# Optimization experiments

Hardware: AMD Instinct MI355X
Metric: run time of the kernel (lower is better)

Reference implementation:

```python
import jax, jax.numpy as jnp
import numpy as np

N_USERS = 50000
N_ITEMS = 100000
N = N_USERS + N_ITEMS
D = 64
N_LAYERS = 3
N_INTENTS = 128
T_SIZE = 32
TEMP = 0.2
KL_REG = 0.01
EMB_REG = 1e-5
INT_REG = 1e-5
SSL_REG = 0.1
B = 4096
E_RAND = 3_000_000


def setup_inputs() -> dict:
    key = jax.random.key(0)
    ks = jax.random.split(key, 12)
    # edge list: random edges + self loops so every node has degree >= 1
    h_rand = jax.random.randint(ks[0], (E_RAND,), 0, N, dtype=jnp.int32)
    t_rand = jax.random.randint(ks[1], (E_RAND,), 0, N, dtype=jnp.int32)
    loops = jnp.arange(N, dtype=jnp.int32)
    h_list = jnp.concatenate([loops, h_rand])
    t_list = jnp.concatenate([loops, t_rand])
    return {
        "user_emb": jax.random.normal(ks[2], (N_USERS, D), jnp.float32) * 0.1,
        "item_emb": jax.random.normal(ks[3], (N_ITEMS, D), jnp.float32) * 0.1,
        "user_intent": jax.random.normal(ks[4], (D, N_INTENTS), jnp.float32) * 0.1,
        "item_intent": jax.random.normal(ks[5], (D, N_INTENTS), jnp.float32) * 0.1,
        "lin_w": jax.random.normal(ks[6], (D, T_SIZE), jnp.float32) * 0.1,
        "lin_b": jnp.zeros((D,), jnp.float32),
        "eps": jax.random.uniform(ks[7], (N, D), jnp.float32),
        "h_list": h_list,
        "t_list": t_list,
        "users": jax.random.randint(ks[8], (B,), 0, N_USERS, dtype=jnp.int32),
        "pos_items": jax.random.randint(ks[9], (B,), 0, N_ITEMS, dtype=jnp.int32),
        "neg_items": jax.random.randint(ks[10], (B,), 0, N_ITEMS, dtype=jnp.int32),
    }


def _normalize(x):
    return x / jnp.linalg.norm(x, axis=1, keepdims=True)


def _infonce(e1, e2):
    pos = jnp.exp(jnp.sum(e1 * e2, axis=1) / TEMP)                 # [B]
    neg = jnp.sum(jnp.exp(e1 @ e2.T / TEMP), axis=1)               # [B]
    return jnp.mean(-jnp.log(pos / (neg + 1e-8) + 1e-8))


def reference(user_emb, item_emb, user_intent, item_intent, lin_w, lin_b,
              eps, h_list, t_list, users, pos_items, neg_items):
    # ---- symmetric normalization D^-1/2 A D^-1/2 (A values = 1) ----
    deg = jax.ops.segment_sum(jnp.ones_like(h_list, dtype=jnp.float32), h_list,
                              num_segments=N)
    d_inv = deg ** -0.5
    g_vals = d_inv[h_list] * d_inv[t_list]                          # [E]

    # ---- multi-layer SpMM propagation, layer-sum aggregation ----
    ego = jnp.concatenate([user_emb, item_emb], axis=0)             # [N, D]
    acc = ego
    cur = ego
    for _ in range(N_LAYERS):
        cur = jax.ops.segment_sum(g_vals[:, None] * cur[t_list], h_list,
                                  num_segments=N)                   # spmm
        acc = acc + cur
    all_emb = acc                                                   # [N, D]
    ua, ia = all_emb[:N_USERS], all_emb[N_USERS:]

    # ---- generative learning ----
    mean = all_emb
    std = jax.nn.softplus(all_emb[:, :T_SIZE])
    std = std @ lin_w.T + lin_b + 1e-8                              # [N, D]
    gen_emb = mean + eps * std

    # ---- intent model ----
    u_int = jax.nn.softmax(ua @ user_intent, axis=1) @ user_intent.T
    i_int = jax.nn.softmax(ia @ item_intent, axis=1) @ item_intent.T

    # ---- BPR loss ----
    u_e = ua[users]
    pos_scores = jnp.sum(u_e * ia[pos_items], axis=1)
    neg_scores = jnp.sum(u_e * ia[neg_items], axis=1)
    bpr_loss = jnp.mean(jax.nn.softplus(neg_scores - pos_scores))

    # ---- KL loss ----
    kl = -0.5 * (1.0 + 2.0 * std - jnp.square(mean) - jnp.exp(2.0 * std))
    kl = jnp.where(jnp.isfinite(kl), kl, 0.0)
    kl_loss = KL_REG * jnp.mean(jnp.sum(kl, axis=1))
    gen_loss = bpr_loss + kl_loss

    # ---- embedding / intent regularizers ----
    emb_loss = EMB_REG * (jnp.sum(jnp.square(user_emb[users]))
                          + jnp.sum(jnp.square(item_emb[pos_items]))
                          + jnp.sum(jnp.square(item_emb[neg_items])))
    int_loss = INT_REG * (jnp.sum(jnp.square(user_intent))
                          + jnp.sum(jnp.square(item_intent)))

    # ---- SSL (InfoNCE) loss ----
    u_gen = _normalize(gen_emb[:N_USERS][users])
    i_gen = _normalize(gen_emb[N_USERS:][pos_items])
    u_i = _normalize(u_int[users])
    i_i = _normalize(i_int[pos_items])
    cl_loss = SSL_REG * (_infonce(u_gen, u_i) + _infonce(i_gen, i_i))

    return (gen_loss, cl_loss, emb_loss, int_loss)
```

## Files before the change

### kernel.cpp

```cpp
#include <hip/hip_runtime.h>

#define NU 50000
#define NI 100000
#define NT 150000
#define BB 4096
#define NBUCK 147
#define BCAP 24576
#define NCH 8
#define KLB 1920

typedef __attribute__((ext_vector_type(8))) short bf16x8;
typedef __attribute__((ext_vector_type(4))) float f32x4;
typedef __attribute__((ext_vector_type(2))) float f32x2;
typedef unsigned long long u64;

__device__ __forceinline__ float softplusf(float x) {
  return fmaxf(x, 0.f) + __logf(1.f + __expf(-fabsf(x)));
}
__device__ __forceinline__ float wsum(float v) {
#pragma unroll
  for (int o = 32; o > 0; o >>= 1) v += __shfl_xor(v, o, 64);
  return v;
}
__device__ __forceinline__ unsigned short f2b(float x) {
  unsigned u = __float_as_uint(x);
  return (unsigned short)((u + 0x7FFFu + ((u >> 16) & 1u)) >> 16);
}
__device__ __forceinline__ float b2f(unsigned us) {
  return __uint_as_float(us << 16);
}
__device__ __forceinline__ float bfe(bf16x8 v, int j) {
  return __uint_as_float(((unsigned)(unsigned short)v[j]) << 16);
}
__device__ __forceinline__ void unp4(u64 v, float* o) {
  unsigned lo = (unsigned)v, hi = (unsigned)(v >> 32);
  o[0] = __uint_as_float(lo << 16);
  o[1] = __uint_as_float(lo & 0xffff0000u);
  o[2] = __uint_as_float(hi << 16);
  o[3] = __uint_as_float(hi & 0xffff0000u);
}
__device__ __forceinline__ u64 pk4(float x0, float x1, float x2, float x3) {
  return (u64)((unsigned)f2b(x0) | ((unsigned)f2b(x1) << 16)) |
         ((u64)((unsigned)f2b(x2) | ((unsigned)f2b(x3) << 16)) << 32);
}
__device__ __forceinline__ f32x2 pkfma(f32x2 a, f32x2 b, f32x2 c) {
  f32x2 d;
  asm("v_pk_fma_f32 %0, %1, %2, %3" : "=v"(d) : "v"(a), "v"(b), "v"(c));
  return d;
}

__global__ void k_zero(int* __restrict__ gcur, float* __restrict__ negu,
                       float* __restrict__ negi) {
  int t = threadIdx.x;
  for (int i = t; i < NBUCK; i += 256) gcur[i] = 0;
  for (int i = t; i < BB; i += 256) { negu[i] = 0.f; negi[i] = 0.f; }
}

__global__ __launch_bounds__(256) void k_part(const int* __restrict__ h,
                                              const int* __restrict__ t,
                                              int* __restrict__ gcur,
                                              uint2* __restrict__ part, int E) {
  __shared__ int cnt[NBUCK];
  __shared__ int base[NBUCK];
  for (int b = threadIdx.x; b < NBUCK; b += 256) cnt[b] = 0;
  __syncthreads();
  int e0 = blockIdx.x * 4096 + threadIdx.x * 16;
  int nval = E - e0;
  nval = nval < 0 ? 0 : (nval > 16 ? 16 : nval);
  int hh[16], tt[16];
  if (nval == 16) {
    const int4* hp = (const int4*)(h + e0);
    const int4* tp = (const int4*)(t + e0);
#pragma unroll
    for (int j = 0; j < 4; j++) {
      int4 v = hp[j];
      hh[j * 4] = v.x; hh[j * 4 + 1] = v.y; hh[j * 4 + 2] = v.z; hh[j * 4 + 3] = v.w;
      int4 w = tp[j];
      tt[j * 4] = w.x; tt[j * 4 + 1] = w.y; tt[j * 4 + 2] = w.z; tt[j * 4 + 3] = w.w;
    }
  } else {
    for (int j = 0; j < nval; j++) { hh[j] = h[e0 + j]; tt[j] = t[e0 + j]; }
  }
  for (int j = 0; j < nval; j++) atomicAdd(&cnt[hh[j] >> 10], 1);
  __syncthreads();
  for (int b = threadIdx.x; b < NBUCK; b += 256) {
    int c = cnt[b];
    base[b] = c ? atomicAdd(&gcur[b], c) : 0;
    cnt[b] = 0;
  }
  __syncthreads();
  for (int j = 0; j < nval; j++) {
    int b = hh[j] >> 10;
    int r = atomicAdd(&cnt[b], 1);
    uint2 v; v.x = (unsigned)hh[j]; v.y = (unsigned)tt[j];
    part[(size_t)b * BCAP + base[b] + r] = v;
  }
}

__global__ __launch_bounds__(256) void k_count2(const uint2* __restrict__ part,
                                                const int* __restrict__ gcur,
                                                int* __restrict__ cnt_chunk) {
  __shared__ int hist[1024];
  int b = blockIdx.x, c = blockIdx.y, tid = threadIdx.x;
  for (int i = tid; i < 1024; i += 256) hist[i] = 0;
  __syncthreads();
  int m = gcur[b];
  int lo = (int)(((long long)m * c) >> 3);
  int hi = (int)(((long long)m * (c + 1)) >> 3);
  const uint2* pp = part + (size_t)b * BCAP;
  for (int i = lo + tid; i < hi; i += 256) atomicAdd(&hist[pp[i].x & 1023], 1);
  __syncthreads();
  for (int i = tid; i < 1024; i += 256)
    cnt_chunk[((((size_t)b << 10) + i) << 3) + c] = hist[i];
}

__global__ __launch_bounds__(256) void k_node(int* __restrict__ cnt_chunk,
                                              int* __restrict__ rloc_g,
                                              float* __restrict__ d_inv,
                                              int* __restrict__ btot) {
  __shared__ int sd[256];
  int b = blockIdx.x, tid = threadIdx.x;
  int n0 = b << 10;
  int pd[4];
  int s = 0;
#pragma unroll
  for (int j = 0; j < 4; j++) {
    int idx = tid * 4 + j;
    size_t base = ((size_t)(n0 + idx)) << 3;
    int run = 0;
#pragma unroll
    for (int c = 0; c < NCH; c++) {
      int v = cnt_chunk[base + c];
      cnt_chunk[base + c] = run;
      run += v;
    }
    int n = n0 + idx;
    if (n < NT) {
      d_inv[n] = 1.0f / sqrtf((float)run);
      pd[j] = run;
    } else pd[j] = 0;
    s += pd[j];
  }
  sd[tid] = s;
  __syncthreads();
  for (int o = 1; o < 256; o <<= 1) {
    int x = (tid >= o) ? sd[tid - o] : 0;
    __syncthreads();
    sd[tid] += x;
    __syncthreads();
  }
  int run2 = sd[tid] - s;
#pragma unroll
  for (int j = 0; j < 4; j++) {
    int idx = tid * 4 + j, n = n0 + idx;
    if (n < NT) rloc_g[n] = run2;
    run2 += pd[j];
  }
  if (tid == 255) btot[b] = sd[255];
}

__global__ __launch_bounds__(256) void k_fill2(const uint2* __restrict__ part,
                                               const int* __restrict__ gcur,
                                               const int* __restrict__ chunkpre,
                                               const int* __restrict__ rloc_g,
                                               const int* __restrict__ btot,
                                               const float* __restrict__ d_inv,
                                               uint2* __restrict__ edges,
                                               int* __restrict__ row_ptr) {
  __shared__ int curs[1024];
  __shared__ float dl[1024];
  __shared__ int sd[256];
  __shared__ int exs[256];
  int b = blockIdx.x, c = blockIdx.y, tid = threadIdx.x;
  int v = (tid < NBUCK) ? btot[tid] : 0;
  sd[tid] = v;
  __syncthreads();
  for (int o = 1; o < 256; o <<= 1) {
    int x = (tid >= o) ? sd[tid - o] : 0;
    __syncthreads();
    sd[tid] += x;
    __syncthreads();
  }
  exs[tid] = sd[tid] - v;
  __syncthreads();
  int exB = exs[b];
  int n0 = b << 10;
  for (int i = tid; i < 1024; i += 256) {
    int n = n0 + i;
    if (n < NT) {
      int rp = exB + rloc_g[n];
      curs[i] = rp + chunkpre[((((size_t)b << 10) + i) << 3) + c];
      dl[i] = d_inv[n];
      if (c == 0) row_ptr[n] = rp;
    }
  }
  if (c == 0 && b == 0 && tid == 0) row_ptr[NT] = exs[255];
  __syncthreads();
  int m = gcur[b];
  int lo = (int)(((long long)m * c) >> 3);
  int hi = (int)(((long long)m * (c + 1)) >> 3);
  const uint2* pp = part + (size_t)b * BCAP;
  for (int i = lo + tid; i < hi; i += 256) {
    uint2 pe = pp[i];
    int slot = atomicAdd(&curs[pe.x & 1023], 1);
    float g = dl[pe.x & 1023] * d_inv[pe.y];
    uint2 w; w.x = pe.y; w.y = __float_as_uint(g);
    edges[slot] = w;
  }
}

__global__ void k_init(const float4* __restrict__ ue, const float4* __restrict__ ie,
                       unsigned* __restrict__ cur, u64* __restrict__ acc64,
                       int nU4, int nTot4) {
  int i = blockIdx.x * 256 + threadIdx.x;
  if (i >= nTot4) return;
  float4 v = (i < nU4) ? ue[i] : ie[i - nU4];
  int p = __builtin_amdgcn_cvt_pk_fp8_f32(v.x, v.y, 0, false);
  p = __builtin_amdgcn_cvt_pk_fp8_f32(v.z, v.w, p, true);
  cur[i] = (unsigned)p;
  acc64[i] = pk4(v.x, v.y, v.z, v.w);
}

__device__ __forceinline__ void agg32(const u64* __restrict__ ep,
                                      const unsigned* __restrict__ cur,
                                      int i, int e, int d, int b4,
                                      f32x2& a01, f32x2& a23) {
  int ia = i + d;
  int ib = ia + 16;
  u64 ra = ep[ia < e ? ia : e - 1];
  u64 rb = ep[ib < e ? ib : e - 1];
  unsigned rax = (unsigned)ra;
  unsigned ray = (ia < e) ? (unsigned)(ra >> 32) : 0u;
  unsigned rbx = (unsigned)rb;
  unsigned rby = (ib < e) ? (unsigned)(rb >> 32) : 0u;
  unsigned iA0 = __shfl(rax, b4 + 0, 64); float gA0 = __uint_as_float(__shfl(ray, b4 + 0, 64));
  unsigned iA1 = __shfl(rax, b4 + 1, 64); float gA1 = __uint_as_float(__shfl(ray, b4 + 1, 64));
  unsigned iA2 = __shfl(rax, b4 + 2, 64); float gA2 = __uint_as_float(__shfl(ray, b4 + 2, 64));
  unsigned iA3 = __shfl(rax, b4 + 3, 64); float gA3 = __uint_as_float(__shfl(ray, b4 + 3, 64));
  unsigned vA0 = cur[(iA0 << 4) + (unsigned)d];
  unsigned vA1 = cur[(iA1 << 4) + (unsigned)d];
  unsigned vA2 = cur[(iA2 << 4) + (unsigned)d];
  unsigned vA3 = cur[(iA3 << 4) + (unsigned)d];
  unsigned iB0 = __shfl(rbx, b4 + 0, 64); float gB0 = __uint_as_float(__shfl(rby, b4 + 0, 64));
  unsigned iB1 = __shfl(rbx, b4 + 1, 64); float gB1 = __uint_as_float(__shfl(rby, b4 + 1, 64));
  unsigned iB2 = __shfl(rbx, b4 + 2, 64); float gB2 = __uint_as_float(__shfl(rby, b4 + 2, 64));
  unsigned iB3 = __shfl(rbx, b4 + 3, 64); float gB3 = __uint_as_float(__shfl(rby, b4 + 3, 64));
  unsigned vB0 = cur[(iB0 << 4) + (unsigned)d];
  unsigned vB1 = cur[(iB1 << 4) + (unsigned)d];
  unsigned vB2 = cur[(iB2 << 4) + (unsigned)d];
  unsigned vB3 = cur[(iB3 << 4) + (unsigned)d];
  f32x2 g2;
  g2.x = gA0; g2.y = gA0;
  a01 = pkfma(__builtin_amdgcn_cvt_pk_f32_fp8(vA0, false), g2, a01);
  a23 = pkfma(__builtin_amdgcn_cvt_pk_f32_fp8(vA0, true), g2, a23);
  g2.x = gA1; g2.y = gA1;
  a01 = pkfma(__builtin_amdgcn_cvt_pk_f32_fp8(vA1, false), g2, a01);
  a23 = pkfma(__builtin_amdgcn_cvt_pk_f32_fp8(vA1, true), g2, a23);
  g2.x = gA2; g2.y = gA2;
  a01 = pkfma(__builtin_amdgcn_cvt_pk_f32_fp8(vA2, false), g2, a01);
  a23 = pkfma(__builtin_amdgcn_cvt_pk_f32_fp8(vA2, true), g2, a23);
  g2.x = gA3; g2.y = gA3;
  a01 = pkfma(__builtin_amdgcn_cvt_pk_f32_fp8(vA3, false), g2, a01);
  a23 = pkfma(__builtin_amdgcn_cvt_pk_f32_fp8(vA3, true), g2, a23);
  g2.x = gB0; g2.y = gB0;
  a01 = pkfma(__builtin_amdgcn_cvt_pk_f32_fp8(vB0, false), g2, a01);
  a23 = pkfma(__builtin_amdgcn_cvt_pk_f32_fp8(vB0, true), g2, a23);
  g2.x = gB1; g2.y = gB1;
  a01 = pkfma(__builtin_amdgcn_cvt_pk_f32_fp8(vB1, false), g2, a01);
  a23 = pkfma(__builtin_amdgcn_cvt_pk_f32_fp8(vB1, true), g2, a23);
  g2.x = gB2; g2.y = gB2;
  a01 = pkfma(__builtin_amdgcn_cvt_pk_f32_fp8(vB2, false), g2, a01);
  a23 = pkfma(__builtin_amdgcn_cvt_pk_f32_fp8(vB2, true), g2, a23);
  g2.x = gB3; g2.y = gB3;
  a01 = pkfma(__builtin_amdgcn_cvt_pk_f32_fp8(vB3, false), g2, a01);
  a23 = pkfma(__builtin_amdgcn_cvt_pk_f32_fp8(vB3, true), g2, a23);
}

__global__ __launch_bounds__(256) void k_agg(const int* __restrict__ row_ptr,
                                             const uint2* __restrict__ edges,
                                             const unsigned* __restrict__ cur,
                                             unsigned* __restrict__ nxt,
                                             u64* __restrict__ acc64,
                                             int last) {
  int node0 = (((blockIdx.x << 2) + (threadIdx.x >> 6)) << 1);
  int node1 = node0 + 1;
  unsigned lane = threadIdx.x & 63;
  int d = (int)(lane & 15);
  int g = (int)(lane >> 4);
  int b4 = g << 2;
  int s0 = row_ptr[node0];
  int e0 = row_ptr[node1];
  int e1 = row_ptr[node1 + 1];
  int s1 = e0;
  f32x2 x01 = {0.f, 0.f}, x23 = {0.f, 0.f};
  f32x2 y01 = {0.f, 0.f}, y23 = {0.f, 0.f};
  const u64* ep = (const u64*)edges;
  int l0 = e0 - s0, l1 = e1 - s1;
  int len = l0 > l1 ? l0 : l1;
  for (int k = 0; k < len; k += 32) {
    agg32(ep, cur, s0 + k, e0, d, b4, x01, x23);
    agg32(ep, cur, s1 + k, e1, d, b4, y01, y23);
  }
  float x0 = x01.x, x1 = x01.y, x2 = x23.x, x3 = x23.y;
  float y0 = y01.x, y1 = y01.y, y2 = y23.x, y3 = y23.y;
  x0 += __shfl_xor(x0, 16, 64); x1 += __shfl_xor(x1, 16, 64);
  x2 += __shfl_xor(x2, 16, 64); x3 += __shfl_xor(x3, 16, 64);
  y0 += __shfl_xor(y0, 16, 64); y1 += __shfl_xor(y1, 16, 64);
  y2 += __shfl_xor(y2, 16, 64); y3 += __shfl_xor(y3, 16, 64);
  x0 += __shfl_xor(x0, 32, 64); x1 += __shfl_xor(x1, 32, 64);
  x2 += __shfl_xor(x2, 32, 64); x3 += __shfl_xor(x3, 32, 64);
  y0 += __shfl_xor(y0, 32, 64); y1 += __shfl_xor(y1, 32, 64);
  y2 += __shfl_xor(y2, 32, 64); y3 += __shfl_xor(y3, 32, 64);
  if (g < 2) {
    int nd = (g == 0) ? node0 : node1;
    float a0 = (g == 0) ? x0 : y0;
    float a1 = (g == 0) ? x1 : y1;
    float a2 = (g == 0) ? x2 : y2;
    float a3 = (g == 0) ? x3 : y3;
    unsigned ro = ((unsigned)nd << 4) + (unsigned)d;
    u64 pv = acc64[ro];
    unsigned lo32 = (unsigned)pv, hi32 = (unsigned)(pv >> 32);
    float z0 = __uint_as_float(lo32 << 16) + a0;
    float z1 = __uint_as_float(lo32 & 0xffff0000u) + a1;
    float z2 = __uint_as_float(hi32 << 16) + a2;
    float z3 = __uint_as_float(hi32 & 0xffff0000u) + a3;
    acc64[ro] = pk4(z0, z1, z2, z3);
  } else if (!last) {
    int nd = (g == 2) ? node0 : node1;
    float a0 = (g == 2) ? x0 : y0;
    float a1 = (g == 2) ? x1 : y1;
    float a2 = (g == 2) ? x2 : y2;
    float a3 = (g == 2) ? x3 : y3;
    unsigned ro = ((unsigned)nd << 4) + (unsigned)d;
    int p = __builtin_amdgcn_cvt_pk_fp8_f32(a0, a1, 0, false);
    p = __builtin_amdgcn_cvt_pk_fp8_f32(a2, a3, p, true);
    nxt[ro] = (unsigned)p;
  }
}

__global__ __launch_bounds__(256) void k_batch(
    const unsigned short* __restrict__ accB,
    const float* __restrict__ user_emb, const float* __restrict__ item_emb,
    const float* __restrict__ eps,
    const float* __restrict__ user_int, const float* __restrict__ item_int,
    const float* __restrict__ lin_w, const float* __restrict__ lin_b,
    const int* __restrict__ users, const int* __restrict__ pos_items,
    const int* __restrict__ neg_items,
    unsigned short* __restrict__ ugen_b, unsigned short* __restrict__ uio_b,
    unsigned short* __restrict__ igen_b, unsigned short* __restrict__ iio_b,
    float* __restrict__ posu, float* __restrict__ posi,
    double* __restrict__ bprp, double* __restrict__ esp) {
  __shared__ __align__(16) unsigned short sUIT[128 * 72];
  __shared__ __align__(16) unsigned short sUI[64 * 136];
  __shared__ __align__(16) unsigned short sP[4][16 * 136];
  __shared__ double red[8];
  int bid = blockIdx.x;
  int lane = threadIdx.x & 63;
  int wid = threadIdx.x >> 6;
  int n = lane & 15, q = lane >> 4;
  int isI = bid >> 6;
  int i0 = ((bid & 63) << 6) + wid * 16;
  const float* intent = isI ? item_int : user_int;
  for (int i = threadIdx.x; i < 8192; i += 256) {
    int dd = i >> 7, kk = i & 127;
    unsigned short v = f2b(intent[i]);
    sUIT[kk * 72 + dd] = v;
    sUI[dd * 136 + kk] = v;
  }
  __syncthreads();
  unsigned short* myP = &sP[wid][0];
  int piN = pos_items[i0 + n];
  int rw = isI ? (NU + piN) : users[i0 + n];
  const unsigned short* arp = accB + (size_t)rw * 64;
  bf16x8 a0 = *(const bf16x8*)(arp + q * 8);
  bf16x8 a1 = *(const bf16x8*)(arp + 32 + q * 8);
  f32x4 c[8];
#pragma unroll
  for (int kt = 0; kt < 8; kt++) {
    const unsigned short* bp = &sUIT[(kt * 16 + n) * 72 + q * 8];
    bf16x8 b0 = *(const bf16x8*)bp;
    bf16x8 b1 = *(const bf16x8*)(bp + 32);
    f32x4 z = {0.f, 0.f, 0.f, 0.f};
    z = __builtin_amdgcn_mfma_f32_16x16x32_bf16(a0, b0, z, 0, 0, 0);
    c[kt] = __builtin_amdgcn_mfma_f32_16x16x32_bf16(a1, b1, z, 0, 0, 0);
  }
  float mx[4], tot[4];
#pragma unroll
  for (int r = 0; r < 4; r++) {
    float m = c[0][r];
#pragma unroll
    for (int kt = 1; kt < 8; kt++) m = fmaxf(m, c[kt][r]);
#pragma unroll
    for (int o = 1; o < 16; o <<= 1) m = fmaxf(m, __shfl_xor(m, o, 64));
    mx[r] = m;
  }
#pragma unroll
  for (int kt = 0; kt < 8; kt++)
#pragma unroll
    for (int r = 0; r < 4; r++) c[kt][r] = __expf(c[kt][r] - mx[r]);
#pragma unroll
  for (int r = 0; r < 4; r++) {
    float t = 0.f;
#pragma unroll
    for (int kt = 0; kt < 8; kt++) t += c[kt][r];
#pragma unroll
    for (int o = 1; o < 16; o <<= 1) t += __shfl_xor(t, o, 64);
    tot[r] = 1.f / t;
  }
#pragma unroll
  for (int kt = 0; kt < 8; kt++)
#pragma unroll
    for (int r = 0; r < 4; r++)
      myP[(q * 4 + r) * 136 + kt * 16 + n] = f2b(c[kt][r] * tot[r]);
  f32x4 s[4];
#pragma unroll
  for (int dt = 0; dt < 4; dt++) s[dt] = (f32x4){0.f, 0.f, 0.f, 0.f};
#pragma unroll
  for (int cc = 0; cc < 4; cc++) {
    bf16x8 pa = *(const bf16x8*)&myP[n * 136 + cc * 32 + q * 8];
#pragma unroll
    for (int dt = 0; dt < 4; dt++) {
      bf16x8 bb = *(const bf16x8*)&sUI[(dt * 16 + n) * 136 + cc * 32 + q * 8];
      s[dt] = __builtin_amdgcn_mfma_f32_16x16x32_bf16(pa, bb, s[dt], 0, 0, 0);
    }
  }
  float rin[4];
#pragma unroll
  for (int r = 0; r < 4; r++) {
    float t = 0.f;
#pragma unroll
    for (int dt = 0; dt < 4; dt++) t += s[dt][r] * s[dt][r];
#pragma unroll
    for (int o = 1; o < 16; o <<= 1) t += __shfl_xor(t, o, 64);
    rin[r] = 1.f / sqrtf(t);
  }
  float iov[4][4];
  unsigned short* iob = isI ? iio_b : uio_b;
#pragma unroll
  for (int dt = 0; dt < 4; dt++)
#pragma unroll
    for (int r = 0; r < 4; r++) {
      float v = s[dt][r] * rin[r];
      iov[dt][r] = v;
      iob[(size_t)(i0 + q * 4 + r) * 64 + dt * 16 + n] = f2b(v);
    }
  bf16x8 A3;
#pragma unroll
  for (int j = 0; j < 8; j++) A3[j] = (short)f2b(softplusf(bfe(a0, j)));
  f32x4 sd4[4];
  float lbv[4];
#pragma unroll
  for (int dt = 0; dt < 4; dt++) {
    const float* wp = lin_w + (size_t)(dt * 16 + n) * 32 + q * 8;
    float4 w0 = *(const float4*)wp;
    float4 w1 = *(const float4*)(wp + 4);
    bf16x8 B3;
    B3[0] = (short)f2b(w0.x); B3[1] = (short)f2b(w0.y);
    B3[2] = (short)f2b(w0.z); B3[3] = (short)f2b(w0.w);
    B3[4] = (short)f2b(w1.x); B3[5] = (short)f2b(w1.y);
    B3[6] = (short)f2b(w1.z); B3[7] = (short)f2b(w1.w);
    f32x4 z = {0.f, 0.f, 0.f, 0.f};
    sd4[dt] = __builtin_amdgcn_mfma_f32_16x16x32_bf16(A3, B3, z, 0, 0, 0);
    lbv[dt] = lin_b[dt * 16 + n];
  }
  *(bf16x8*)&myP[n * 136 + q * 8] = a0;
  *(bf16x8*)&myP[n * 136 + 32 + q * 8] = a1;
  int rwr[4];
#pragma unroll
  for (int r = 0; r < 4; r++) rwr[r] = __shfl(rw, q * 4 + r, 64);
  float ge[4][4];
#pragma unroll
  for (int dt = 0; dt < 4; dt++)
#pragma unroll
    for (int r = 0; r < 4; r++) {
      float mcv = b2f(myP[(q * 4 + r) * 136 + dt * 16 + n]);
      float ep = eps[(size_t)rwr[r] * 64 + dt * 16 + n];
      float sdf = sd4[dt][r] + lbv[dt] + 1e-8f;
      ge[dt][r] = mcv + ep * sdf;
    }
  float gin[4];
#pragma unroll
  for (int r = 0; r < 4; r++) {
    float t = 0.f;
#pragma unroll
    for (int dt = 0; dt < 4; dt++) t += ge[dt][r] * ge[dt][r];
#pragma unroll
    for (int o = 1; o < 16; o <<= 1) t += __shfl_xor(t, o, 64);
    gin[r] = 1.f / sqrtf(t);
  }
  float pd[4] = {0.f, 0.f, 0.f, 0.f};
  unsigned short* gob = isI ? igen_b : ugen_b;
#pragma unroll
  for (int dt = 0; dt < 4; dt++)
#pragma unroll
    for (int r = 0; r < 4; r++) {
      float go = ge[dt][r] * gin[r];
      gob[(size_t)(i0 + q * 4 + r) * 64 + dt * 16 + n] = f2b(go);
      pd[r] = fmaf(go, iov[dt][r], pd[r]);
    }
  float* posX = isI ? posi : posu;
#pragma unroll
  for (int r = 0; r < 4; r++) {
    float t = pd[r];
#pragma unroll
    for (int o = 1; o < 16; o <<= 1) t += __shfl_xor(t, o, 64);
    if (n == 0) posX[i0 + q * 4 + r] = t;
  }
  if (!isI) {
    int niN = neg_items[i0 + n];
    const unsigned short* pp = accB + (size_t)(NU + piN) * 64;
    const unsigned short* np = accB + (size_t)(NU + niN) * 64;
    bf16x8 p0 = *(const bf16x8*)(pp + q * 8);
    bf16x8 p1 = *(const bf16x8*)(pp + 32 + q * 8);
    bf16x8 n0 = *(const bf16x8*)(np + q * 8);
    bf16x8 n1 = *(const bf16x8*)(np + 32 + q * 8);
    float ps = 0.f, ns = 0.f;
#pragma unroll
    for (int j = 0; j < 8; j++) {
      float m0 = bfe(a0, j), m1 = bfe(a1, j);
      ps = fmaf(m0, bfe(p0, j), ps); ps = fmaf(m1, bfe(p1, j), ps);
      ns = fmaf(m0, bfe(n0, j), ns); ns = fmaf(m1, bfe(n1, j), ns);
    }
    ps += __shfl_xor(ps, 16, 64); ps += __shfl_xor(ps, 32, 64);
    ns += __shfl_xor(ns, 16, 64); ns += __shfl_xor(ns, 32, 64);
    float bpr = softplusf(ns - ps);
    const float* uep = user_emb + (size_t)rw * 64 + q * 16;
    float es = 0.f;
#pragma unroll
    for (int j = 0; j < 4; j++) {
      float4 u4 = *(const float4*)(uep + j * 4);
      es += u4.x * u4.x + u4.y * u4.y + u4.z * u4.z + u4.w * u4.w;
    }
    es += __shfl_xor(es, 16, 64); es += __shfl_xor(es, 32, 64);
#pragma unroll
    for (int o = 1; o < 16; o <<= 1) {
      bpr += __shfl_xor(bpr, o, 64);
      es += __shfl_xor(es, o, 64);
    }
    if (lane == 0) { red[wid] = (double)bpr; red[4 + wid] = (double)es; }
    __syncthreads();
    if (threadIdx.x == 0) {
      bprp[bid] = red[0] + red[1] + red[2] + red[3];
      esp[bid] = red[4] + red[5] + red[6] + red[7];
    }
  } else {
    int niN = neg_items[i0 + n];
    const float* pe = item_emb + (size_t)piN * 64 + q * 16;
    const float* ne = item_emb + (size_t)niN * 64 + q * 16;
    float es = 0.f;
#pragma unroll
    for (int j = 0; j < 4; j++) {
      float4 u4 = *(const float4*)(pe + j * 4);
      float4 v4 = *(const float4*)(ne + j * 4);
      es += u4.x * u4.x + u4.y * u4.y + u4.z * u4.z + u4.w * u4.w;
      es += v4.x * v4.x + v4.y * v4.y + v4.z * v4.z + v4.w * v4.w;
    }
    es += __shfl_xor(es, 16, 64); es += __shfl_xor(es, 32, 64);
#pragma unroll
    for (int o = 1; o < 16; o <<= 1) es += __shfl_xor(es, o, 64);
    if (lane == 0) red[wid] = (double)es;
    __syncthreads();
    if (threadIdx.x == 0)
      esp[bid] = red[0] + red[1] + red[2] + red[3];
  }
}

__global__ __launch_bounds__(256) void k_nk(
    const unsigned short* __restrict__ e1u, const unsigned short* __restrict__ e2u,
    const unsigned short* __restrict__ e1i, const unsigned short* __restrict__ e2i,
    float* __restrict__ negu, float* __restrict__ negi,
    const unsigned short* __restrict__ accB,
    const float* __restrict__ lin_w, const float* __restrict__ lin_b,
    const float* __restrict__ user_int, const float* __restrict__ item_int,
    double* __restrict__ klp, double* __restrict__ intp) {
  __shared__ double red[4];
  __shared__ __align__(16) uint4 sE2[2048];
  int bid = blockIdx.x;
  int lane = threadIdx.x & 63;
  int wid = threadIdx.x >> 6;
  int n = lane & 15, q = lane >> 4;
  if (bid < 2048) {
    int bx = bid & 63, by = bid >> 6;
    int pr = by >> 4, jq = by & 15;
    const unsigned short* e1 = pr ? e1i : e1u;
    const unsigned short* e2 = pr ? e2i : e2u;
    float* nego = pr ? negi : negu;
    const uint4* e2v = (const uint4*)e2 + (size_t)jq * 2048;
#pragma unroll
    for (int k = 0; k < 8; k++) {
      int i = (int)threadIdx.x + k * 256;
      int row = i >> 3, cch = i & 7;
      sE2[(i & ~7) | (cch ^ (row & 7))] = e2v[i];
    }
    int i0 = bx * 64 + wid * 16;
    const bf16x8* arow = (const bf16x8*)(e1 + (size_t)(i0 + n) * 64 + q * 8);
    bf16x8 a0 = arow[0];
    bf16x8 a1 = arow[4];
    __syncthreads();
    f32x4 accv = {0.f, 0.f, 0.f, 0.f};
    int sw = n & 7;
    for (int jt = 0; jt < 16; jt += 2) {
      int r0 = jt * 16 + n;
      const uint4* base0 = &sE2[r0 * 8];
      const uint4* base1 = &sE2[(r0 + 16) * 8];
      bf16x8 b0 = *(const bf16x8*)&base0[q ^ sw];
      bf16x8 b1 = *(const bf16x8*)&base0[(q + 4) ^ sw];
      bf16x8 b2 = *(const bf16x8*)&base1[q ^ sw];
      bf16x8 b3 = *(const bf16x8*)&base1[(q + 4) ^ sw];
      f32x4 c = {0.f, 0.f, 0.f, 0.f};
      f32x4 c2 = {0.f, 0.f, 0.f, 0.f};
      c = __builtin_amdgcn_mfma_f32_16x16x32_bf16(a0, b0, c, 0, 0, 0);
      c = __builtin_amdgcn_mfma_f32_16x16x32_bf16(a1, b1, c, 0, 0, 0);
      c2 = __builtin_amdgcn_mfma_f32_16x16x32_bf16(a0, b2, c2, 0, 0, 0);
      c2 = __builtin_amdgcn_mfma_f32_16x16x32_bf16(a1, b3, c2, 0, 0, 0);
#pragma unroll
      for (int r = 0; r < 4; r++)
        accv[r] += __expf(5.0f * c[r]) + __expf(5.0f * c2[r]);
    }
#pragma unroll
    for (int o = 1; o < 16; o <<= 1) {
#pragma unroll
      for (int r = 0; r < 4; r++) accv[r] += __shfl_xor(accv[r], o, 64);
    }
    if (n == 0) {
#pragma unroll
      for (int r = 0; r < 4; r++) atomicAdd(&nego[i0 + q * 4 + r], accv[r]);
    }
  } else if (bid < 2048 + KLB) {
    bf16x8 B0, B1, B2, B3;
    float lb0, lb1, lb2, lb3;
    {
      const float* w0 = lin_w + (0 * 16 + n) * 32 + q * 8;
      const float* w1 = lin_w + (1 * 16 + n) * 32 + q * 8;
      const float* w2 = lin_w + (2 * 16 + n) * 32 + q * 8;
      const float* w3 = lin_w + (3 * 16 + n) * 32 + q * 8;
#pragma unroll
      for (int j = 0; j < 8; j++) {
        B0[j] = (short)f2b(w0[j]);
        B1[j] = (short)f2b(w1[j]);
        B2[j] = (short)f2b(w2[j]);
        B3[j] = (short)f2b(w3[j]);
      }
      lb0 = lin_b[0 * 16 + n] + 1e-8f;
      lb1 = lin_b[1 * 16 + n] + 1e-8f;
      lb2 = lin_b[2 * 16 + n] + 1e-8f;
      lb3 = lin_b[3 * 16 + n] + 1e-8f;
    }
    const int TI = NT / 16;
    int w0id = (bid - 2048) * 4 + wid;
    int nwv = KLB * 4;
    double dsum = 0.0;
    for (int tile = w0id; tile < TI; tile += nwv) {
      const uint4* rp = (const uint4*)(accB + (size_t)(tile * 16 + n) * 64 + q * 8);
      uint4 A = rp[0];
      uint4 C = rp[4];
      u64 A0 = ((u64)A.y << 32) | A.x;
      u64 A1 = ((u64)A.w << 32) | A.z;
      u64 C0 = ((u64)C.y << 32) | C.x;
      u64 C1 = ((u64)C.w << 32) | C.z;
      float av[8], bv[8];
      unp4(A0, av); unp4(A1, av + 4);
      unp4(C0, bv); unp4(C1, bv + 4);
      float msum = 0.f;
#pragma unroll
      for (int j = 0; j < 8; j++) msum += av[j] * av[j] + bv[j] * bv[j];
      bf16x8 Af;
#pragma unroll
      for (int j = 0; j < 8; j++) Af[j] = (short)f2b(softplusf(av[j]));
      f32x4 z = {0.f, 0.f, 0.f, 0.f};
      f32x4 c0 = __builtin_amdgcn_mfma_f32_16x16x32_bf16(Af, B0, z, 0, 0, 0);
      f32x4 c1 = __builtin_amdgcn_mfma_f32_16x16x32_bf16(Af, B1, z, 0, 0, 0);
      f32x4 c2 = __builtin_amdgcn_mfma_f32_16x16x32_bf16(Af, B2, z, 0, 0, 0);
      f32x4 c3 = __builtin_amdgcn_mfma_f32_16x16x32_bf16(Af, B3, z, 0, 0, 0);
      float ksum = 0.f;
#pragma unroll
      for (int r = 0; r < 4; r++) {
        float s0 = c0[r] + lb0, s1 = c1[r] + lb1, s2 = c2[r] + lb2, s3 = c3[r] + lb3;
        ksum += -0.5f * (1.f + 2.f * s0 - __expf(2.f * s0));
        ksum += -0.5f * (1.f + 2.f * s1 - __expf(2.f * s1));
        ksum += -0.5f * (1.f + 2.f * s2 - __expf(2.f * s2));
        ksum += -0.5f * (1.f + 2.f * s3 - __expf(2.f * s3));
      }
      dsum += (double)wsum(ksum + 0.5f * msum);
    }
    if (lane == 0) red[wid] = dsum;
    __syncthreads();
    if (threadIdx.x == 0)
      klp[bid - 2048] = red[0] + red[1] + red[2] + red[3];
  } else {
    float s = 0.f;
    for (int i = threadIdx.x; i < 64 * 128; i += 256) {
      float a = user_int[i], b = item_int[i];
      s = fmaf(a, a, s);
      s = fmaf(b, b, s);
    }
    s = wsum(s);
    if (lane == 0) red[wid] = (double)s;
    __syncthreads();
    if (threadIdx.x == 0)
      intp[0] = red[0] + red[1] + red[2] + red[3];
  }
}

__global__ __launch_bounds__(256) void k_out(
    const float* __restrict__ posu, const float* __restrict__ posi,
    const float* __restrict__ negu, const float* __restrict__ negi,
    const double* __restrict__ bprp, const double* __restrict__ esp,
    const double* __restrict__ klp, const double* __restrict__ intp,
    float* __restrict__ out) {
  __shared__ double redd[16];
  int tid = threadIdx.x;
  int lane = tid & 63, wid = tid >> 6;
  double cl = 0.0;
  for (int i = tid; i < 2 * BB; i += 256) {
    int pr = i >> 12, idx = i & (BB - 1);
    float ng = pr ? negi[idx] : negu[idx];
    float dt = pr ? posi[idx] : posu[idx];
    float pos = expf(5.0f * dt);
    cl += (double)(-logf(pos / (ng + 1e-8f) + 1e-8f));
  }
  double kl = 0.0;
  for (int i = tid; i < KLB; i += 256) kl += klp[i];
  double bpr = (tid < 64) ? bprp[tid] : 0.0;
  double es = (tid < 128) ? esp[tid] : 0.0;
#pragma unroll
  for (int o = 32; o > 0; o >>= 1) {
    cl += __shfl_xor(cl, o, 64);
    kl += __shfl_xor(kl, o, 64);
    bpr += __shfl_xor(bpr, o, 64);
    es += __shfl_xor(es, o, 64);
  }
  if (lane == 0) {
    redd[wid] = cl; redd[4 + wid] = kl;
    redd[8 + wid] = bpr; redd[12 + wid] = es;
  }
  __syncthreads();
  if (tid == 0) {
    double cls = redd[0] + redd[1] + redd[2] + redd[3];
    double kls = redd[4] + redd[5] + redd[6] + redd[7];
    double bprs = redd[8] + redd[9] + redd[10] + redd[11];
    double ess = redd[12] + redd[13] + redd[14] + redd[15];
    out[0] = (float)(bprs / (double)BB + 0.01 * kls / (double)NT);
    out[1] = (float)(0.1 * cls / (double)BB);
    out[2] = (float)(1e-5 * ess);
    out[3] = (float)(1e-5 * intp[0]);
  }
}

extern "C" void kernel_launch(void* const* d_in, const int* in_sizes, int n_in,
                              void* d_out, int out_size, void* d_ws, size_t ws_size,
                              hipStream_t stream) {
  const float* user_emb = (const float*)d_in[0];
  const float* item_emb = (const float*)d_in[1];
  const float* user_int = (const float*)d_in[2];
  const float* item_int = (const float*)d_in[3];
  const float* lin_w = (const float*)d_in[4];
  const float* lin_b = (const float*)d_in[5];
  const float* eps = (const float*)d_in[6];
  const int* h_list = (const int*)d_in[7];
  const int* t_list = (const int*)d_in[8];
  const int* users = (const int*)d_in[9];
  const int* pos_items = (const int*)d_in[10];
  const int* neg_items = (const int*)d_in[11];
  float* out = (float*)d_out;
  const int E = in_sizes[7];

  char* ws = (char*)d_ws;
  size_t off = 0;
  auto take = [&](size_t bytes) -> char* {
    char* p = ws + off;
    off = (off + bytes + 255) & ~(size_t)255;
    return p;
  };
  int* row_ptr = (int*)take((size_t)(NT + 1) * 4);
  float* d_inv = (float*)take((size_t)NT * 4);
  int* rloc_g = (int*)take((size_t)NT * 4);
  int* cnt_chunk = (int*)take((size_t)NBUCK * NCH * 1024 * 4);
  int* gcur = (int*)take(NBUCK * 4);
  int* btot = (int*)take(NBUCK * 4);
  uint2* edges = (uint2*)take((size_t)E * 8);
  unsigned* bufA = (unsigned*)take((size_t)NT * 16 * 4);
  unsigned* bufB = (unsigned*)take((size_t)NT * 16 * 4);
  unsigned short* accB = (unsigned short*)take((size_t)NBUCK * BCAP * 8);
  unsigned short* ugen_b = (unsigned short*)take((size_t)BB * 64 * 2);
  unsigned short* igen_b = (unsigned short*)take((size_t)BB * 64 * 2);
  unsigned short* uio_b = (unsigned short*)take((size_t)BB * 64 * 2);
  unsigned short* iio_b = (unsigned short*)take((size_t)BB * 64 * 2);
  float* posu = (float*)take((size_t)BB * 4);
  float* posi = (float*)take((size_t)BB * 4);
  float* negu = (float*)take((size_t)BB * 4);
  float* negi = (float*)take((size_t)BB * 4);
  double* klp = (double*)take((size_t)KLB * 8);
  double* bprp = (double*)take(64 * 8);
  double* esp = (double*)take(128 * 8);
  double* intp = (double*)take(8);
  if (off > ws_size) return;
  uint2* part = (uint2*)accB;
  u64* acc64 = (u64*)accB;

  k_zero<<<1, 256, 0, stream>>>(gcur, negu, negi);

  int gridP = (E + 4095) / 4096;
  k_part<<<gridP, 256, 0, stream>>>(h_list, t_list, gcur, part, E);
  k_count2<<<dim3(NBUCK, NCH), 256, 0, stream>>>(part, gcur, cnt_chunk);
  k_node<<<NBUCK, 256, 0, stream>>>(cnt_chunk, rloc_g, d_inv, btot);
  k_fill2<<<dim3(NBUCK, NCH), 256, 0, stream>>>(part, gcur, cnt_chunk, rloc_g,
                                                btot, d_inv, edges, row_ptr);

  int nU4 = NU * 16, nTot4 = NT * 16;
  k_init<<<(nTot4 + 255) / 256, 256, 0, stream>>>((const float4*)user_emb,
                                                  (const float4*)item_emb, bufA,
                                                  acc64, nU4, nTot4);
  int gridAgg = NT / 8;
  k_agg<<<gridAgg, 256, 0, stream>>>(row_ptr, edges, bufA, bufB, acc64, 0);
  k_agg<<<gridAgg, 256, 0, stream>>>(row_ptr, edges, bufB, bufA, acc64, 0);
  k_agg<<<gridAgg, 256, 0, stream>>>(row_ptr, edges, bufA, bufB, acc64, 1);

  k_batch<<<128, 256, 0, stream>>>(accB, user_emb, item_emb, eps,
                                   user_int, item_int, lin_w, lin_b,
                                   users, pos_items, neg_items,
                                   ugen_b, uio_b, igen_b, iio_b,
                                   posu, posi, bprp, esp);
  k_nk<<<2048 + KLB + 1, 256, 0, stream>>>(ugen_b, uio_b, igen_b, iio_b,
                                           negu, negi, accB, lin_w, lin_b,
                                           user_int, item_int, klp, intp);
  k_out<<<1, 256, 0, stream>>>(posu, posi, negu, negi, bprp, esp, klp, intp,
                               out);
}
```

Before: 423.1 us.

## Replace bucketed CSR build with global-atomic degree count, scan, and scatter

Replaces the two-pass bucket partition (k_part, k_count2, k_node, k_fill2) with a direct CSR build. Global atomic degree counting is followed by a two-level scan into row pointers and cursors, then each edge is scattered with a global atomicAdd on its row cursor. This drops the intermediate partition buffer and a pass over the edges, but adds heavy random global atomics and uncoalesced scattered writes over 3.15M edges. The edge order within each row becomes nondeterministic. The aggregation loop also skips agg32 calls once a node's edge list is exhausted.

```diff
diff --git a/kernel.cpp b/kernel.cpp
--- a/kernel.cpp
+++ b/kernel.cpp
@@ -3,10 +3,8 @@
 #define NU 50000
 #define NI 100000
 #define NT 150000
+#define NTP 150528
 #define BB 4096
-#define NBUCK 147
-#define BCAP 24576
-#define NCH 8
 #define KLB 1920
 
 typedef __attribute__((ext_vector_type(8))) short bf16x8;
@@ -49,97 +47,34 @@
   return d;
 }
 
-__global__ void k_zero(int* __restrict__ gcur, float* __restrict__ negu,
-                       float* __restrict__ negi) {
-  int t = threadIdx.x;
-  for (int i = t; i < NBUCK; i += 256) gcur[i] = 0;
-  for (int i = t; i < BB; i += 256) { negu[i] = 0.f; negi[i] = 0.f; }
-}
-
-__global__ __launch_bounds__(256) void k_part(const int* __restrict__ h,
-                                              const int* __restrict__ t,
-                                              int* __restrict__ gcur,
-                                              uint2* __restrict__ part, int E) {
-  __shared__ int cnt[NBUCK];
-  __shared__ int base[NBUCK];
-  for (int b = threadIdx.x; b < NBUCK; b += 256) cnt[b] = 0;
-  __syncthreads();
-  int e0 = blockIdx.x * 4096 + threadIdx.x * 16;
-  int nval = E - e0;
-  nval = nval < 0 ? 0 : (nval > 16 ? 16 : nval);
-  int hh[16], tt[16];
-  if (nval == 16) {
-    const int4* hp = (const int4*)(h + e0);
-    const int4* tp = (const int4*)(t + e0);
-#pragma unroll
-    for (int j = 0; j < 4; j++) {
-      int4 v = hp[j];
-      hh[j * 4] = v.x; hh[j * 4 + 1] = v.y; hh[j * 4 + 2] = v.z; hh[j * 4 + 3] = v.w;
-      int4 w = tp[j];
-      tt[j * 4] = w.x; tt[j * 4 + 1] = w.y; tt[j * 4 + 2] = w.z; tt[j * 4 + 3] = w.w;
-    }
+__global__ __launch_bounds__(256) void k_deg(const int* __restrict__ h,
+                                             int* __restrict__ deg, int E) {
+  int i0 = (blockIdx.x * 256 + threadIdx.x) * 4;
+  if (i0 + 3 < E) {
+    int4 v = *(const int4*)(h + i0);
+    atomicAdd(&deg[v.x], 1);
+    atomicAdd(&deg[v.y], 1);
+    atomicAdd(&deg[v.z], 1);
+    atomicAdd(&deg[v.w], 1);
   } else {
-    for (int j = 0; j < nval; j++) { hh[j] = h[e0 + j]; tt[j] = t[e0 + j]; }
-  }
-  for (int j = 0; j < nval; j++) atomicAdd(&cnt[hh[j] >> 10], 1);
-  __syncthreads();
-  for (int b = threadIdx.x; b < NBUCK; b += 256) {
-    int c = cnt[b];
-    base[b] = c ? atomicAdd(&gcur[b], c) : 0;
-    cnt[b] = 0;
-  }
-  __syncthreads();
-  for (int j = 0; j < nval; j++) {
-    int b = hh[j] >> 10;
-    int r = atomicAdd(&cnt[b], 1);
-    uint2 v; v.x = (unsigned)hh[j]; v.y = (unsigned)tt[j];
-    part[(size_t)b * BCAP + base[b] + r] = v;
-  }
-}
-
-__global__ __launch_bounds__(256) void k_count2(const uint2* __restrict__ part,
-                                                const int* __restrict__ gcur,
-                                                int* __restrict__ cnt_chunk) {
-  __shared__ int hist[1024];
-  int b = blockIdx.x, c = blockIdx.y, tid = threadIdx.x;
-  for (int i = tid; i < 1024; i += 256) hist[i] = 0;
-  __syncthreads();
-  int m = gcur[b];
-  int lo = (int)(((long long)m * c) >> 3);
-  int hi = (int)(((long long)m * (c + 1)) >> 3);
-  const uint2* pp = part + (size_t)b * BCAP;
-  for (int i = lo + tid; i < hi; i += 256) atomicAdd(&hist[pp[i].x & 1023], 1);
-  __syncthreads();
-  for (int i = tid; i < 1024; i += 256)
-    cnt_chunk[((((size_t)b << 10) + i) << 3) + c] = hist[i];
-}
-
-__global__ __launch_bounds__(256) void k_node(int* __restrict__ cnt_chunk,
-                                              int* __restrict__ rloc_g,
-                                              float* __restrict__ d_inv,
-                                              int* __restrict__ btot) {
+    for (int j = i0; j < E; j++) atomicAdd(&deg[h[j]], 1);
+  }
+}
+
+__global__ __launch_bounds__(256) void k_scan1(const int* __restrict__ deg,
+                                               int* __restrict__ rloc_g,
+                                               float* __restrict__ d_inv,
+                                               int* __restrict__ btot) {
   __shared__ int sd[256];
   int b = blockIdx.x, tid = threadIdx.x;
   int n0 = b << 10;
-  int pd[4];
-  int s = 0;
+  int4 dv = ((const int4*)(deg + n0))[tid];
+  int pd[4] = {dv.x, dv.y, dv.z, dv.w};
+  int s = pd[0] + pd[1] + pd[2] + pd[3];
 #pragma unroll
   for (int j = 0; j < 4; j++) {
-    int idx = tid * 4 + j;
-    size_t base = ((size_t)(n0 + idx)) << 3;
-    int run = 0;
-#pragma unroll
-    for (int c = 0; c < NCH; c++) {
-      int v = cnt_chunk[base + c];
-      cnt_chunk[base + c] = run;
-      run += v;
-    }
-    int n = n0 + idx;
-    if (n < NT) {
-      d_inv[n] = 1.0f / sqrtf((float)run);
-      pd[j] = run;
-    } else pd[j] = 0;
-    s += pd[j];
+    int n = n0 + tid * 4 + j;
+    if (n < NT) d_inv[n] = 1.0f / sqrtf((float)pd[j]);
   }
   sd[tid] = s;
   __syncthreads();
@@ -152,60 +87,65 @@
   int run2 = sd[tid] - s;
 #pragma unroll
   for (int j = 0; j < 4; j++) {
-    int idx = tid * 4 + j, n = n0 + idx;
-    if (n < NT) rloc_g[n] = run2;
+    rloc_g[n0 + tid * 4 + j] = run2;
     run2 += pd[j];
   }
   if (tid == 255) btot[b] = sd[255];
 }
 
-__global__ __launch_bounds__(256) void k_fill2(const uint2* __restrict__ part,
-                                               const int* __restrict__ gcur,
-                                               const int* __restrict__ chunkpre,
+__global__ __launch_bounds__(256) void k_scan2(const int* __restrict__ btot,
                                                const int* __restrict__ rloc_g,
-                                               const int* __restrict__ btot,
-                                               const float* __restrict__ d_inv,
-                                               uint2* __restrict__ edges,
-                                               int* __restrict__ row_ptr) {
-  __shared__ int curs[1024];
-  __shared__ float dl[1024];
+                                               int* __restrict__ row_ptr,
+                                               int* __restrict__ cursor) {
   __shared__ int sd[256];
   __shared__ int exs[256];
-  int b = blockIdx.x, c = blockIdx.y, tid = threadIdx.x;
-  int v = (tid < NBUCK) ? btot[tid] : 0;
-  sd[tid] = v;
+  int t = threadIdx.x;
+  int v = (t < 147) ? btot[t] : 0;
+  sd[t] = v;
   __syncthreads();
   for (int o = 1; o < 256; o <<= 1) {
-    int x = (tid >= o) ? sd[tid - o] : 0;
-    __syncthreads();
-    sd[tid] += x;
-    __syncthreads();
-  }
-  exs[tid] = sd[tid] - v;
+    int x = (t >= o) ? sd[t - o] : 0;
+    __syncthreads();
+    sd[t] += x;
+    __syncthreads();
+  }
+  exs[t] = sd[t] - v;
   __syncthreads();
-  int exB = exs[b];
-  int n0 = b << 10;
-  for (int i = tid; i < 1024; i += 256) {
-    int n = n0 + i;
-    if (n < NT) {
-      int rp = exB + rloc_g[n];
-      curs[i] = rp + chunkpre[((((size_t)b << 10) + i) << 3) + c];
-      dl[i] = d_inv[n];
-      if (c == 0) row_ptr[n] = rp;
-    }
-  }
-  if (c == 0 && b == 0 && tid == 0) row_ptr[NT] = exs[255];
-  __syncthreads();
-  int m = gcur[b];
-  int lo = (int)(((long long)m * c) >> 3);
-  int hi = (int)(((long long)m * (c + 1)) >> 3);
-  const uint2* pp = part + (size_t)b * BCAP;
-  for (int i = lo + tid; i < hi; i += 256) {
-    uint2 pe = pp[i];
-    int slot = atomicAdd(&curs[pe.x & 1023], 1);
-    float g = dl[pe.x & 1023] * d_inv[pe.y];
-    uint2 w; w.x = pe.y; w.y = __float_as_uint(g);
-    edges[slot] = w;
+  int n = blockIdx.x * 256 + t;
+  if (n < NT) {
+    int rp = exs[n >> 10] + rloc_g[n];
+    row_ptr[n] = rp;
+    cursor[n] = rp;
+  }
+  if (blockIdx.x == 0 && t == 0) row_ptr[NT] = sd[146];
+}
+
+__global__ __launch_bounds__(256) void k_place(const int* __restrict__ h,
+                                               const int* __restrict__ t,
+                                               int* __restrict__ cursor,
+                                               const float* __restrict__ d_inv,
+                                               uint2* __restrict__ edges, int E) {
+  int i0 = (blockIdx.x * 256 + threadIdx.x) * 4;
+  if (i0 + 3 < E) {
+    int4 hv = *(const int4*)(h + i0);
+    int4 tv = *(const int4*)(t + i0);
+#pragma unroll
+    for (int j = 0; j < 4; j++) {
+      int hh = (j == 0) ? hv.x : (j == 1) ? hv.y : (j == 2) ? hv.z : hv.w;
+      int tt = (j == 0) ? tv.x : (j == 1) ? tv.y : (j == 2) ? tv.z : tv.w;
+      int slot = atomicAdd(&cursor[hh], 1);
+      float g = d_inv[hh] * d_inv[tt];
+      uint2 w; w.x = (unsigned)tt; w.y = __float_as_uint(g);
+      edges[slot] = w;
+    }
+  } else {
+    for (int j = i0; j < E; j++) {
+      int hh = h[j], tt = t[j];
+      int slot = atomicAdd(&cursor[hh], 1);
+      float g = d_inv[hh] * d_inv[tt];
+      uint2 w; w.x = (unsigned)tt; w.y = __float_as_uint(g);
+      edges[slot] = w;
+    }
   }
 }
 
@@ -298,8 +238,8 @@
   int l0 = e0 - s0, l1 = e1 - s1;
   int len = l0 > l1 ? l0 : l1;
   for (int k = 0; k < len; k += 32) {
-    agg32(ep, cur, s0 + k, e0, d, b4, x01, x23);
-    agg32(ep, cur, s1 + k, e1, d, b4, y01, y23);
+    if (k < l0) agg32(ep, cur, s0 + k, e0, d, b4, x01, x23);
+    if (k < l1) agg32(ep, cur, s1 + k, e1, d, b4, y01, y23);
   }
   float x0 = x01.x, x1 = x01.y, x2 = x23.x, x3 = x23.y;
   float y0 = y01.x, y1 = y01.y, y2 = y23.x, y3 = y23.y;
@@ -772,40 +712,39 @@
     off = (off + bytes + 255) & ~(size_t)255;
     return p;
   };
+  char* zws = take((size_t)NTP * 4 + (size_t)BB * 4 * 2);
+  int* deg = (int*)zws;
+  float* negu = (float*)(zws + (size_t)NTP * 4);
+  float* negi = negu + BB;
   int* row_ptr = (int*)take((size_t)(NT + 1) * 4);
-  float* d_inv = (float*)take((size_t)NT * 4);
-  int* rloc_g = (int*)take((size_t)NT * 4);
-  int* cnt_chunk = (int*)take((size_t)NBUCK * NCH * 1024 * 4);
-  int* gcur = (int*)take(NBUCK * 4);
-  int* btot = (int*)take(NBUCK * 4);
+  float* d_inv = (float*)take((size_t)NTP * 4);
+  int* rloc_g = (int*)take((size_t)NTP * 4);
+  int* cursor = (int*)take((size_t)NTP * 4);
+  int* btot = (int*)take(147 * 4);
   uint2* edges = (uint2*)take((size_t)E * 8);
   unsigned* bufA = (unsigned*)take((size_t)NT * 16 * 4);
   unsigned* bufB = (unsigned*)take((size_t)NT * 16 * 4);
-  unsigned short* accB = (unsigned short*)take((size_t)NBUCK * BCAP * 8);
+  unsigned short* accB = (unsigned short*)take((size_t)NT * 64 * 2);
   unsigned short* ugen_b = (unsigned short*)take((size_t)BB * 64 * 2);
   unsigned short* igen_b = (unsigned short*)take((size_t)BB * 64 * 2);
   unsigned short* uio_b = (unsigned short*)take((size_t)BB * 64 * 2);
   unsigned short* iio_b = (unsigned short*)take((size_t)BB * 64 * 2);
   float* posu = (float*)take((size_t)BB * 4);
   float* posi = (float*)take((size_t)BB * 4);
-  float* negu = (float*)take((size_t)BB * 4);
-  float* negi = (float*)take((size_t)BB * 4);
   double* klp = (double*)take((size_t)KLB * 8);
   double* bprp = (double*)take(64 * 8);
   double* esp = (double*)take(128 * 8);
   double* intp = (double*)take(8);
   if (off > ws_size) return;
-  uint2* part = (uint2*)accB;
   u64* acc64 = (u64*)accB;
 
-  k_zero<<<1, 256, 0, stream>>>(gcur, negu, negi);
-
-  int gridP = (E + 4095) / 4096;
-  k_part<<<gridP, 256, 0, stream>>>(h_list, t_list, gcur, part, E);
-  k_count2<<<dim3(NBUCK, NCH), 256, 0, stream>>>(part, gcur, cnt_chunk);
-  k_node<<<NBUCK, 256, 0, stream>>>(cnt_chunk, rloc_g, d_inv, btot);
-  k_fill2<<<dim3(NBUCK, NCH), 256, 0, stream>>>(part, gcur, cnt_chunk, rloc_g,
-                                                btot, d_inv, edges, row_ptr);
+  hipMemsetAsync(zws, 0, (size_t)NTP * 4 + (size_t)BB * 4 * 2, stream);
+
+  int gridE = (E + 1023) / 1024;
+  k_deg<<<gridE, 256, 0, stream>>>(h_list, deg, E);
+  k_scan1<<<147, 256, 0, stream>>>(deg, rloc_g, d_inv, btot);
+  k_scan2<<<(NT + 255) / 256, 256, 0, stream>>>(btot, rloc_g, row_ptr, cursor);
+  k_place<<<gridE, 256, 0, stream>>>(h_list, t_list, cursor, d_inv, edges, E);
 
   int nU4 = NU * 16, nTot4 = NT * 16;
   k_init<<<(nTot4 + 255) / 256, 256, 0, stream>>>((const float4*)user_emb,
```

Measured after the change: 589.7 us. +39.4%, slower.
